# Performance work log

Hardware: AMD Instinct MI355X
Metric: run time of the kernel (lower is better)

Reference implementation:

```python
import jax, jax.numpy as jnp
import numpy as np

NUM_QUERIES = 300


def setup_inputs() -> dict:
    key = jax.random.key(0)
    ks = jax.random.split(key, 16)
    B, C, NC = 16, 256, 80
    s = 0.02
    return {
        "s3": jax.random.normal(ks[0], (B, C, 128, 128), jnp.float32),
        "s4": jax.random.normal(ks[1], (B, C, 64, 64), jnp.float32),
        "s5": jax.random.normal(ks[2], (B, C, 32, 32), jnp.float32),
        "w_score": jax.random.normal(ks[3], (C, NC), jnp.float32) * s,
        "b_score": jnp.zeros((NC,), jnp.float32),
        "w1": jax.random.normal(ks[4], (C, C), jnp.float32) * s,
        "b1": jnp.zeros((C,), jnp.float32),
        "w2": jax.random.normal(ks[5], (C, C), jnp.float32) * s,
        "b2": jnp.zeros((C,), jnp.float32),
        "w3": jax.random.normal(ks[6], (C, 4), jnp.float32) * s,
        "b3": jnp.zeros((4,), jnp.float32),
        "w_proj": jax.random.normal(ks[7], (C, C), jnp.float32) * s,
        "b_proj": jnp.zeros((C,), jnp.float32),
    }


def _flatten(feats):
    # each feat [B,C,H,W] -> [B,H*W,C]; concat over levels
    mems = [f.reshape(f.shape[0], f.shape[1], -1).transpose(0, 2, 1) for f in feats]
    return jnp.concatenate(mems, axis=1)


def reference(s3, s4, s5, w_score, b_score, w1, b1, w2, b2, w3, b3, w_proj, b_proj):
    memory = _flatten([s3, s4, s5])  # [B, N, C]

    # encoder heads
    enc_logits = memory @ w_score + b_score                      # [B, N, num_classes]
    h = jax.nn.relu(memory @ w1 + b1)
    h = jax.nn.relu(h @ w2 + b2)
    enc_boxes = h @ w3 + b3                                      # [B, N, 4]

    # top-k query selection: sigmoid -> per-token max class score -> topk -> gather
    scores = jax.nn.sigmoid(enc_logits).max(axis=-1)             # [B, N]
    topk_scores, topk_idx = jax.lax.top_k(scores, NUM_QUERIES)   # [B, K]
    topk_mem = jnp.take_along_axis(memory, topk_idx[:, :, None], axis=1)    # [B, K, C]
    topk_boxes = jnp.take_along_axis(enc_boxes, topk_idx[:, :, None], axis=1)  # [B, K, 4]

    tgt = topk_mem @ w_proj + b_proj                             # [B, K, C]
    ref_points = jax.nn.sigmoid(topk_boxes)                      # [B, K, 4]

    return (tgt, ref_points, enc_logits, jax.nn.sigmoid(enc_boxes), topk_idx, topk_scores)
```

## Files before the change

kernel.cpp:

```cpp
#include <hip/hip_runtime.h>
#include <math.h>

#define BATCH 16
#define CDIM 256
#define NCLS 80
#define N3 16384
#define N4 4096
#define N5 1024
#define NTOK 21504
#define KQ 300
#define KSEL 512
#define CANDMAX 1024

typedef __attribute__((ext_vector_type(8))) short short8;
typedef __attribute__((ext_vector_type(4))) float floatx4;
typedef unsigned short ushort_t;

__device__ __forceinline__ float sigmoidf_(float x) {
    return 1.0f / (1.0f + __expf(-x));
}

__device__ __forceinline__ ushort_t f2bf(float f) {
    unsigned int x = __float_as_uint(f);
    unsigned int r = (x + 0x7FFFu + ((x >> 16) & 1u)) >> 16;
    return (ushort_t)r;
}

__device__ __forceinline__ void gload16(const void* g, void* l) {
    __builtin_amdgcn_global_load_lds(
        (const __attribute__((address_space(1))) unsigned int*)g,
        (__attribute__((address_space(3))) unsigned int*)l,
        16, 0, 0);
}

__device__ __forceinline__ void locate_level(
    int n, int bb,
    const float* __restrict__ s3, const float* __restrict__ s4, const float* __restrict__ s5,
    const float*& src, int& nloc, int& lsz)
{
    if (n < N3)           { src = s3 + (size_t)bb * CDIM * N3; nloc = n;           lsz = N3; }
    else if (n < N3 + N4) { src = s4 + (size_t)bb * CDIM * N4; nloc = n - N3;      lsz = N4; }
    else                  { src = s5 + (size_t)bb * CDIM * N5; nloc = n - N3 - N4; lsz = N5; }
}

__global__ __launch_bounds__(256) void prep_weights(
    const float* __restrict__ w1, const float* __restrict__ w2,
    const float* __restrict__ w_score,
    ushort_t* __restrict__ w1T, ushort_t* __restrict__ w2T, ushort_t* __restrict__ wsT)
{
    const int k = threadIdx.x;
    const int c = blockIdx.x;
    const int klo = k & 7;
    if (c < 256) {
        const size_t d = (size_t)c * 256 + ((((k >> 3) ^ (c & 7)) << 3) | klo);
        w1T[d] = f2bf(w1[k * 256 + c]);
    } else if (c < 512) {
        const int c2 = c - 256;
        const size_t d = (size_t)c2 * 256 + ((((k >> 3) ^ (c2 & 7)) << 3) | klo);
        w2T[d] = f2bf(w2[k * 256 + c2]);
    } else {
        const int c2 = c - 512;
        const size_t d = (size_t)c2 * 256 + ((((k >> 3) ^ (c2 & 7)) << 3) | klo);
        wsT[d] = (c2 < NCLS) ? f2bf(w_score[k * NCLS + c2]) : (ushort_t)0;
    }
}

__global__ __launch_bounds__(256, 2) void enc_mfma_kernel(
    const float* __restrict__ s3, const float* __restrict__ s4, const float* __restrict__ s5,
    const ushort_t* __restrict__ w1T, const ushort_t* __restrict__ w2T,
    const ushort_t* __restrict__ wsT,
    const float* __restrict__ b_score, const float* __restrict__ b1,
    const float* __restrict__ b2,
    const float* __restrict__ w3, const float* __restrict__ b3,
    float* __restrict__ out_logits, float* __restrict__ out_sboxes,
    float* __restrict__ ws_scores)
{
    __shared__ __align__(16) ushort_t ldsA[256 * 68];
    __shared__ __align__(16) ushort_t wbufL[2][32 * 256];
    __shared__ float bsc_s[96];
    __shared__ float b1_s[256];
    __shared__ float b2_s[256];
    __shared__ __align__(16) float w3_s[256 * 4];

    const int t = threadIdx.x;
    const int lane = t & 63;
    const int w = t >> 6;
    const int ml = lane & 15;
    const int quad = lane >> 4;
    const int kq = quad * 8;
    const int m8 = ml & 7;

    const int bb = blockIdx.x / 336;
    const int tile = blockIdx.x % 336;
    const int T0 = tile * 64;

    auto stage_async = [&](const ushort_t* wg, int dbuf) {
        const char* g = (const char*)wg + w * 1024 + (lane << 4);
        char* l = (char*)&wbufL[dbuf][0] + w * 1024;
        #pragma unroll
        for (int i = 0; i < 4; ++i)
            gload16(g + i * 4096, l + i * 4096);
    };

    stage_async(wsT, 0);

    if (t < 96) bsc_s[t] = b_score[t];
    b1_s[t] = b1[t];
    b2_s[t] = b2[t];
    *(float4*)&w3_s[t * 4] = *(const float4*)(w3 + t * 4);

    const float* src; int nloc, lsz;
    locate_level(T0, bb, s3, s4, s5, src, nloc, lsz);

    {
        const int tokq = t & 15;
        const int kr = t >> 4;
        #pragma unroll
        for (int p = 0; p < 16; ++p) {
            const int k = p * 16 + kr;
            const float4 v = *(const float4*)(src + (size_t)k * lsz + nloc + 4 * tokq);
            const unsigned int lo = (unsigned int)f2bf(v.x) | ((unsigned int)f2bf(v.y) << 16);
            const unsigned int hi = (unsigned int)f2bf(v.z) | ((unsigned int)f2bf(v.w) << 16);
            *(uint2*)&ldsA[k * 68 + 4 * tokq] = make_uint2(lo, hi);
        }
    }
    __syncthreads();

    short8 af[8];
    #pragma unroll
    for (int f = 0; f < 8; ++f) {
        short8 a;
        #pragma unroll
        for (int j = 0; j < 8; ++j)
            a[j] = (short)ldsA[(32 * f + kq + j) * 68 + 16 * w + ml];
        af[f] = a;
    }

    const int tokl0 = 16 * w + quad * 4;
    const int tokg0 = bb * NTOK + T0 + tokl0;

    float smax[4] = {-1e30f, -1e30f, -1e30f, -1e30f};
    float psum[4][4];
    #pragma unroll
    for (int r = 0; r < 4; ++r)
        #pragma unroll
        for (int c = 0; c < 4; ++c) psum[r][c] = 0.f;

    int cur = 0;
    for (int i = 0; i < 19; ++i) {
        if (i + 1 < 19) {
            const int j = i + 1;
            const ushort_t* nxt = (j < 3)  ? (wsT + (size_t)j * 8192)
                                : (j < 11) ? (w1T + (size_t)(j - 3) * 8192)
                                           : (w2T + (size_t)(j - 11) * 8192);
            stage_async(nxt, cur ^ 1);
        }

        if (i == 11) {
            #pragma unroll
            for (int f = 0; f < 8; ++f)
                af[f] = *(const short8*)&ldsA[(16 * w + ml) * 264 + 32 * f + kq];
        }

        const ushort_t* wb = &wbufL[cur][0];
        #pragma unroll
        for (int tt = 0; tt < 2; ++tt) {
            if (i < 3 && (2 * i + tt) >= 5) continue;
            const int row = 16 * tt + ml;
            floatx4 acc = {0.f, 0.f, 0.f, 0.f};
            #pragma unroll
            for (int f = 0; f < 8; ++f) {
                const short8 bf = *(const short8*)&wb[row * 256 + (((4 * f + quad) ^ m8) << 3)];
                acc = __builtin_amdgcn_mfma_f32_16x16x32_bf16(af[f], bf, acc, 0, 0, 0);
            }
            if (i < 3) {
                const int col = 16 * (2 * i + tt) + ml;
                const float bias = bsc_s[col];
                #pragma unroll
                for (int r = 0; r < 4; ++r) {
                    const float v = acc[r] + bias;
                    out_logits[(size_t)(tokg0 + r) * NCLS + col] = v;
                    smax[r] = fmaxf(smax[r], v);
                }
            } else if (i < 11) {
                const int col = 32 * (i - 3) + 16 * tt + ml;
                const float bias = b1_s[col];
                #pragma unroll
                for (int r = 0; r < 4; ++r) {
                    const float v = fmaxf(acc[r] + bias, 0.f);
                    ldsA[(tokl0 + r) * 264 + col] = f2bf(v);
                }
            } else {
                const int col = 32 * (i - 11) + 16 * tt + ml;
                const float bias = b2_s[col];
                const float4 w3v = *(const float4*)&w3_s[col * 4];
                #pragma unroll
                for (int r = 0; r < 4; ++r) {
                    const float v = fmaxf(acc[r] + bias, 0.f);
                    psum[r][0] = fmaf(v, w3v.x, psum[r][0]);
                    psum[r][1] = fmaf(v, w3v.y, psum[r][1]);
                    psum[r][2] = fmaf(v, w3v.z, psum[r][2]);
                    psum[r][3] = fmaf(v, w3v.w, psum[r][3]);
                }
            }
        }

        if (i == 2) {
            #pragma unroll
            for (int r = 0; r < 4; ++r) {
                float m = smax[r];
                m = fmaxf(m, __shfl_xor(m, 1));
                m = fmaxf(m, __shfl_xor(m, 2));
                m = fmaxf(m, __shfl_xor(m, 4));
                m = fmaxf(m, __shfl_xor(m, 8));
                smax[r] = m;
            }
            if (ml == 0) {
                #pragma unroll
                for (int r = 0; r < 4; ++r)
                    ws_scores[bb * NTOK + T0 + 16 * w + quad * 4 + r] = sigmoidf_(smax[r]);
            }
        }

        __syncthreads();
        cur ^= 1;
    }

    #pragma unroll
    for (int r = 0; r < 4; ++r)
        #pragma unroll
        for (int c = 0; c < 4; ++c) {
            float v = psum[r][c];
            v += __shfl_xor(v, 1);
            v += __shfl_xor(v, 2);
            v += __shfl_xor(v, 4);
            v += __shfl_xor(v, 8);
            psum[r][c] = v;
        }
    if (ml == 0) {
        #pragma unroll
        for (int r = 0; r < 4; ++r) {
            float4 o;
            o.x = sigmoidf_(psum[r][0] + b3[0]);
            o.y = sigmoidf_(psum[r][1] + b3[1]);
            o.z = sigmoidf_(psum[r][2] + b3[2]);
            o.w = sigmoidf_(psum[r][3] + b3[3]);
            *(float4*)&out_sboxes[(size_t)(bb * NTOK + T0 + 16 * w + quad * 4 + r) * 4] = o;
        }
    }
}

__global__ __launch_bounds__(1024) void select_kernel(
    const float* __restrict__ scores,
    int* __restrict__ cand_idx, unsigned int* __restrict__ cand_cnt)
{
    const int bb = blockIdx.x;
    const int t = threadIdx.x;
    const int lane = t & 63;
    const float* s = scores + bb * NTOK;

    __shared__ unsigned int hist[256];
    __shared__ unsigned int prefix_s, rem_s, cnt_s;

    unsigned int prefix = 0, mask = 0;
    int remaining = KSEL;
    for (int pass = 0; pass < 4; pass++) {
        const int shift = 24 - 8 * pass;
        if (t < 256) hist[t] = 0;
        __syncthreads();
        for (int n = t; n < NTOK; n += 1024) {
            const unsigned int key = __float_as_uint(s[n]);
            const bool pred = ((key & mask) == prefix);
            const unsigned int bin = (key >> shift) & 255u;
            unsigned long long alive = __ballot(pred);
            while (alive) {
                const int leader = __builtin_ctzll(alive);
                const unsigned int lbin = (unsigned int)__shfl((int)bin, leader);
                const unsigned long long match = alive & __ballot(bin == lbin);
                if (lane == leader)
                    atomicAdd(&hist[lbin], (unsigned int)__popcll(match));
                alive &= ~match;
            }
        }
        __syncthreads();
        if (t == 0) {
            int rem = remaining; unsigned int bsel = 0;
            for (int bin = 255; bin >= 0; bin--) {
                int c = (int)hist[bin];
                if (c >= rem) { bsel = (unsigned int)bin; break; }
                rem -= c;
            }
            prefix_s = prefix | (bsel << shift);
            rem_s = (unsigned int)rem;
        }
        __syncthreads();
        prefix = prefix_s; remaining = (int)rem_s;
        mask |= 0xFFu << shift;
        __syncthreads();
    }
    const unsigned int Tkey = prefix;

    if (t == 0) cnt_s = 0;
    __syncthreads();
    for (int n = t; n < NTOK; n += 1024) {
        const unsigned int key = __float_as_uint(s[n]);
        const bool pred = (key >= Tkey);
        const unsigned long long m = __ballot(pred);
        if (m) {
            const int leader = __builtin_ctzll(m);
            unsigned int base = 0;
            if (lane == leader) base = atomicAdd(&cnt_s, (unsigned int)__popcll(m));
            base = (unsigned int)__shfl((int)base, leader);
            if (pred) {
                const unsigned int pos =
                    base + (unsigned int)__popcll(m & ((1ull << lane) - 1ull));
                if (pos < CANDMAX) cand_idx[bb * CANDMAX + pos] = n;
            }
        }
    }
    __syncthreads();
    if (t == 0) {
        unsigned int c = cnt_s; if (c > CANDMAX) c = CANDMAX;
        cand_cnt[bb] = c;
    }
}

__global__ __launch_bounds__(256) void rescore_kernel(
    const float* __restrict__ s3, const float* __restrict__ s4, const float* __restrict__ s5,
    const float* __restrict__ w_score, const float* __restrict__ b_score,
    const int* __restrict__ cand_idx, const unsigned int* __restrict__ cand_cnt,
    double* __restrict__ cand_score)
{
    __shared__ float mrow[4][CDIM];
    const int t = threadIdx.x;
    const int w = t >> 6;
    const int lane = t & 63;
    const int bb = blockIdx.x / (CANDMAX / 4);
    const int c  = (blockIdx.x % (CANDMAX / 4)) * 4 + w;
    const unsigned int cnt = cand_cnt[bb];
    const bool active = (unsigned int)c < cnt;

    int n = 0;
    if (active) n = cand_idx[bb * CANDMAX + c];
    if (active) {
        const float* src; int nloc, lsz;
        locate_level(n, bb, s3, s4, s5, src, nloc, lsz);
        #pragma unroll
        for (int j = 0; j < 4; j++)
            mrow[w][4 * lane + j] = src[(size_t)(4 * lane + j) * lsz + nloc];
    }
    __syncthreads();

    if (active) {
        double acc0 = (double)b_score[lane];
        double acc1 = (lane < 16) ? (double)b_score[64 + lane] : -1.0e300;
        for (int k = 0; k < CDIM; k++) {
            const double m = (double)mrow[w][k];
            acc0 += m * (double)w_score[k * NCLS + lane];
            if (lane < 16) acc1 += m * (double)w_score[k * NCLS + 64 + lane];
        }
        double mx = fmax(acc0, acc1);
        mx = fmax(mx, __shfl_xor(mx, 1));
        mx = fmax(mx, __shfl_xor(mx, 2));
        mx = fmax(mx, __shfl_xor(mx, 4));
        mx = fmax(mx, __shfl_xor(mx, 8));
        mx = fmax(mx, __shfl_xor(mx, 16));
        mx = fmax(mx, __shfl_xor(mx, 32));
        if (lane == 0) cand_score[bb * CANDMAX + c] = mx;
    }
}

__global__ __launch_bounds__(256) void fsort_kernel(
    const double* __restrict__ cand_score, const int* __restrict__ cand_idx,
    const unsigned int* __restrict__ cand_cnt,
    float* __restrict__ out_idx_f, float* __restrict__ out_scores,
    int* __restrict__ ws_idx)
{
    __shared__ double ss[CANDMAX];
    __shared__ int    ii[CANDMAX];
    const int bb = blockIdx.x;
    const int t = threadIdx.x;
    const unsigned int cnt = cand_cnt[bb];

    for (int i = t; i < CANDMAX; i += 256) {
        if ((unsigned int)i < cnt) {
            ss[i] = cand_score[bb * CANDMAX + i];
            ii[i] = cand_idx[bb * CANDMAX + i];
        } else {
            ss[i] = -1.0e300;
            ii[i] = 0x7FFFFFFF;
        }
    }
    __syncthreads();

    for (int ksz = 2; ksz <= CANDMAX; ksz <<= 1) {
        for (int j = ksz >> 1; j > 0; j >>= 1) {
            #pragma unroll
            for (int p = 0; p < CANDMAX / 256; p++) {
                const int i = p * 256 + t;
                const int ixj = i ^ j;
                if (ixj > i) {
                    double sa = ss[i], sb = ss[ixj];
                    int ia = ii[i], ib = ii[ixj];
                    const bool up = ((i & ksz) != 0);
                    const bool agtb = (sa > sb) || (sa == sb && ia < ib);
                    if (agtb == up) { ss[i] = sb; ss[ixj] = sa; ii[i] = ib; ii[ixj] = ia; }
                }
            }
            __syncthreads();
        }
    }

    for (int q = t; q < KQ; q += 256) {
        const double x = ss[q];
        const int idx = ii[q];
        out_scores[bb * KQ + q] = (float)(1.0 / (1.0 + exp(-x)));
        out_idx_f[bb * KQ + q] = (float)idx;
        ws_idx[bb * KQ + q] = idx;
    }
}

__global__ __launch_bounds__(256) void gather_proj_kernel(
    const float* __restrict__ s3, const float* __restrict__ s4, const float* __restrict__ s5,
    const float* __restrict__ w_proj, const float* __restrict__ b_proj,
    const int* __restrict__ ws_idx, const float* __restrict__ out_sboxes,
    float* __restrict__ out_tgt, float* __restrict__ out_ref)
{
    __shared__ float memQ[20][CDIM];
    __shared__ int qidx[20];
    const int t = threadIdx.x;
    const int bb = blockIdx.x / 15;
    const int tile = blockIdx.x % 15;
    const int q0 = tile * 20;

    if (t < 20) qidx[t] = ws_idx[bb * KQ + q0 + t];
    __syncthreads();

    #pragma unroll 4
    for (int q = 0; q < 20; q++) {
        const int n = qidx[q];
        const float* src; int nloc, lsz;
        locate_level(n, bb, s3, s4, s5, src, nloc, lsz);
        memQ[q][t] = src[(size_t)t * lsz + nloc];
    }
    __syncthreads();

    const int j = t;
    float acc[20];
    #pragma unroll
    for (int q = 0; q < 20; q++) acc[q] = b_proj[j];
    for (int k = 0; k < CDIM; k++) {
        const float w = w_proj[(size_t)k * CDIM + j];
        #pragma unroll
        for (int q = 0; q < 20; q++) acc[q] = fmaf(memQ[q][k], w, acc[q]);
    }
    #pragma unroll
    for (int q = 0; q < 20; q++)
        out_tgt[(size_t)(bb * KQ + q0 + q) * CDIM + j] = acc[q];

    if (t < 80) {
        const int q = t >> 2, c = t & 3;
        const int n = qidx[q];
        out_ref[(size_t)(bb * KQ + q0 + q) * 4 + c] =
            out_sboxes[(size_t)(bb * NTOK + n) * 4 + c];
    }
}

extern "C" void kernel_launch(void* const* d_in, const int* in_sizes, int n_in,
                              void* d_out, int out_size, void* d_ws, size_t ws_size,
                              hipStream_t stream) {
    const float* s3      = (const float*)d_in[0];
    const float* s4      = (const float*)d_in[1];
    const float* s5      = (const float*)d_in[2];
    const float* w_score = (const float*)d_in[3];
    const float* b_score = (const float*)d_in[4];
    const float* w1      = (const float*)d_in[5];
    const float* b1      = (const float*)d_in[6];
    const float* w2      = (const float*)d_in[7];
    const float* b2      = (const float*)d_in[8];
    const float* w3      = (const float*)d_in[9];
    const float* b3      = (const float*)d_in[10];
    const float* w_proj  = (const float*)d_in[11];
    const float* b_proj  = (const float*)d_in[12];

    float* out = (float*)d_out;
    float* out_tgt    = out;
    float* out_ref    = out + 1228800;
    float* out_logits = out + 1248000;
    float* out_sboxes = out + 28773120;
    float* out_idx    = out + 30149376;
    float* out_scores = out + 30154176;

    char* ws = (char*)d_ws;
    float*        ws_scores  = (float*)(ws + 0);
    double*       cand_score = (double*)(ws + 1376256);
    int*          cand_idx   = (int*)(ws + 1507328);
    unsigned int* cand_cnt   = (unsigned int*)(ws + 1572864);
    int*          ws_idx     = (int*)(ws + 1573120);
    ushort_t*     w1T        = (ushort_t*)(ws + 1592576);
    ushort_t*     w2T        = (ushort_t*)(ws + 1723648);
    ushort_t*     wsT        = (ushort_t*)(ws + 1854720);

    prep_weights<<<608, 256, 0, stream>>>(w1, w2, w_score, w1T, w2T, wsT);

    enc_mfma_kernel<<<BATCH * 336, 256, 0, stream>>>(
        s3, s4, s5, w1T, w2T, wsT, b_score, b1, b2, w3, b3,
        out_logits, out_sboxes, ws_scores);

    select_kernel<<<BATCH, 1024, 0, stream>>>(ws_scores, cand_idx, cand_cnt);

    rescore_kernel<<<BATCH * (CANDMAX / 4), 256, 0, stream>>>(
        s3, s4, s5, w_score, b_score, cand_idx, cand_cnt, cand_score);

    fsort_kernel<<<BATCH, 256, 0, stream>>>(
        cand_score, cand_idx, cand_cnt, out_idx, out_scores, ws_idx);

    gather_proj_kernel<<<BATCH * 15, 256, 0, stream>>>(
        s3, s4, s5, w_proj, b_proj, ws_idx, out_sboxes, out_tgt, out_ref);
}
```

Baseline: 956.4 us.

## Restructure encoder MLP to 32x32 MFMA with direct global weight fragments

The encoder kernel moves from 16x16x32 MFMA tiles with double-buffered LDS weight staging and per-step barriers to 32x32x16 MFMA tiles. Weights are pre-packed into MFMA fragment order and read straight from global/L2 memory, and the four waves split into two token halves by two column groups. The box head becomes a separate LDS pass after layer two, and select_kernel drops from 1024 to 256 threads with a simpler histogram update. This removes LDS weight staging and many syncs, but every block now re-reads weights from global memory and the register footprint grows.

```diff
diff --git a/kernel.cpp b/kernel.cpp
--- a/kernel.cpp
+++ b/kernel.cpp
@@ -14,6 +14,7 @@
 
 typedef __attribute__((ext_vector_type(8))) short short8;
 typedef __attribute__((ext_vector_type(4))) float floatx4;
+typedef __attribute__((ext_vector_type(16))) float floatx16;
 typedef unsigned short ushort_t;
 
 __device__ __forceinline__ float sigmoidf_(float x) {
@@ -26,11 +27,8 @@
     return (ushort_t)r;
 }
 
-__device__ __forceinline__ void gload16(const void* g, void* l) {
-    __builtin_amdgcn_global_load_lds(
-        (const __attribute__((address_space(1))) unsigned int*)g,
-        (__attribute__((address_space(3))) unsigned int*)l,
-        16, 0, 0);
+__device__ __forceinline__ float bf2f(ushort_t u) {
+    return __uint_as_float((unsigned int)u << 16);
 }
 
 __device__ __forceinline__ void locate_level(
@@ -46,29 +44,32 @@
 __global__ __launch_bounds__(256) void prep_weights(
     const float* __restrict__ w1, const float* __restrict__ w2,
     const float* __restrict__ w_score,
-    ushort_t* __restrict__ w1T, ushort_t* __restrict__ w2T, ushort_t* __restrict__ wsT)
-{
-    const int k = threadIdx.x;
+    ushort_t* __restrict__ wPk)
+{
     const int c = blockIdx.x;
-    const int klo = k & 7;
-    if (c < 256) {
-        const size_t d = (size_t)c * 256 + ((((k >> 3) ^ (c & 7)) << 3) | klo);
-        w1T[d] = f2bf(w1[k * 256 + c]);
-    } else if (c < 512) {
-        const int c2 = c - 256;
-        const size_t d = (size_t)c2 * 256 + ((((k >> 3) ^ (c2 & 7)) << 3) | klo);
-        w2T[d] = f2bf(w2[k * 256 + c2]);
-    } else {
-        const int c2 = c - 512;
-        const size_t d = (size_t)c2 * 256 + ((((k >> 3) ^ (c2 & 7)) << 3) | klo);
-        wsT[d] = (c2 < NCLS) ? f2bf(w_score[k * NCLS + c2]) : (ushort_t)0;
-    }
-}
-
-__global__ __launch_bounds__(256, 2) void enc_mfma_kernel(
+    for (int i = threadIdx.x; i < 8192; i += 256) {
+        const int f = i >> 9;
+        const int e = i & 511;
+        const int ln = e >> 3;
+        const int j = e & 7;
+        const int col = ln & 31;
+        const int k = 16 * f + (ln >> 5) * 8 + j;
+        float v;
+        if (c < 3) {
+            const int cc = 32 * c + col;
+            v = (cc < NCLS) ? w_score[k * NCLS + cc] : 0.f;
+        } else if (c < 11) {
+            v = w1[k * 256 + (32 * (c - 3) + col)];
+        } else {
+            v = w2[k * 256 + (32 * (c - 11) + col)];
+        }
+        wPk[(size_t)c * 8192 + i] = f2bf(v);
+    }
+}
+
+__global__ __launch_bounds__(256) void enc_mfma_kernel(
     const float* __restrict__ s3, const float* __restrict__ s4, const float* __restrict__ s5,
-    const ushort_t* __restrict__ w1T, const ushort_t* __restrict__ w2T,
-    const ushort_t* __restrict__ wsT,
+    const ushort_t* __restrict__ wPk,
     const float* __restrict__ b_score, const float* __restrict__ b1,
     const float* __restrict__ b2,
     const float* __restrict__ w3, const float* __restrict__ b3,
@@ -76,38 +77,20 @@
     float* __restrict__ ws_scores)
 {
     __shared__ __align__(16) ushort_t ldsA[256 * 68];
-    __shared__ __align__(16) ushort_t wbufL[2][32 * 256];
-    __shared__ float bsc_s[96];
-    __shared__ float b1_s[256];
-    __shared__ float b2_s[256];
     __shared__ __align__(16) float w3_s[256 * 4];
+    __shared__ float smax_s[2][64];
 
     const int t = threadIdx.x;
     const int lane = t & 63;
     const int w = t >> 6;
-    const int ml = lane & 15;
-    const int quad = lane >> 4;
-    const int kq = quad * 8;
-    const int m8 = ml & 7;
+    const int tw = w & 1;
+    const int cw = w >> 1;
+    const int ln = lane & 31;
+    const int half = lane >> 5;
 
     const int bb = blockIdx.x / 336;
     const int tile = blockIdx.x % 336;
     const int T0 = tile * 64;
-
-    auto stage_async = [&](const ushort_t* wg, int dbuf) {
-        const char* g = (const char*)wg + w * 1024 + (lane << 4);
-        char* l = (char*)&wbufL[dbuf][0] + w * 1024;
-        #pragma unroll
-        for (int i = 0; i < 4; ++i)
-            gload16(g + i * 4096, l + i * 4096);
-    };
-
-    stage_async(wsT, 0);
-
-    if (t < 96) bsc_s[t] = b_score[t];
-    b1_s[t] = b1[t];
-    b2_s[t] = b2[t];
-    *(float4*)&w3_s[t * 4] = *(const float4*)(w3 + t * 4);
 
     const float* src; int nloc, lsz;
     locate_level(T0, bb, s3, s4, s5, src, nloc, lsz);
@@ -123,134 +106,137 @@
             const unsigned int hi = (unsigned int)f2bf(v.z) | ((unsigned int)f2bf(v.w) << 16);
             *(uint2*)&ldsA[k * 68 + 4 * tokq] = make_uint2(lo, hi);
         }
-    }
-    __syncthreads();
-
-    short8 af[8];
+        *(float4*)&w3_s[t * 4] = *(const float4*)(w3 + t * 4);
+    }
+    __syncthreads();
+
+    short8 af[16];
     #pragma unroll
-    for (int f = 0; f < 8; ++f) {
+    for (int f = 0; f < 16; ++f) {
         short8 a;
         #pragma unroll
         for (int j = 0; j < 8; ++j)
-            a[j] = (short)ldsA[(32 * f + kq + j) * 68 + 16 * w + ml];
+            a[j] = (short)ldsA[(16 * f + 8 * half + j) * 68 + 32 * tw + ln];
         af[f] = a;
     }
-
-    const int tokl0 = 16 * w + quad * 4;
-    const int tokg0 = bb * NTOK + T0 + tokl0;
-
-    float smax[4] = {-1e30f, -1e30f, -1e30f, -1e30f};
-    float psum[4][4];
+    __syncthreads();
+
+    const int gtok0 = bb * NTOK + T0 + 32 * tw;
+
+    float smaxr[16];
     #pragma unroll
-    for (int r = 0; r < 4; ++r)
-        #pragma unroll
-        for (int c = 0; c < 4; ++c) psum[r][c] = 0.f;
-
-    int cur = 0;
-    for (int i = 0; i < 19; ++i) {
-        if (i + 1 < 19) {
-            const int j = i + 1;
-            const ushort_t* nxt = (j < 3)  ? (wsT + (size_t)j * 8192)
-                                : (j < 11) ? (w1T + (size_t)(j - 3) * 8192)
-                                           : (w2T + (size_t)(j - 11) * 8192);
-            stage_async(nxt, cur ^ 1);
-        }
-
-        if (i == 11) {
-            #pragma unroll
-            for (int f = 0; f < 8; ++f)
-                af[f] = *(const short8*)&ldsA[(16 * w + ml) * 264 + 32 * f + kq];
-        }
-
-        const ushort_t* wb = &wbufL[cur][0];
-        #pragma unroll
-        for (int tt = 0; tt < 2; ++tt) {
-            if (i < 3 && (2 * i + tt) >= 5) continue;
-            const int row = 16 * tt + ml;
-            floatx4 acc = {0.f, 0.f, 0.f, 0.f};
-            #pragma unroll
-            for (int f = 0; f < 8; ++f) {
-                const short8 bf = *(const short8*)&wb[row * 256 + (((4 * f + quad) ^ m8) << 3)];
-                acc = __builtin_amdgcn_mfma_f32_16x16x32_bf16(af[f], bf, acc, 0, 0, 0);
-            }
-            if (i < 3) {
-                const int col = 16 * (2 * i + tt) + ml;
-                const float bias = bsc_s[col];
-                #pragma unroll
-                for (int r = 0; r < 4; ++r) {
-                    const float v = acc[r] + bias;
-                    out_logits[(size_t)(tokg0 + r) * NCLS + col] = v;
-                    smax[r] = fmaxf(smax[r], v);
-                }
-            } else if (i < 11) {
-                const int col = 32 * (i - 3) + 16 * tt + ml;
-                const float bias = b1_s[col];
-                #pragma unroll
-                for (int r = 0; r < 4; ++r) {
-                    const float v = fmaxf(acc[r] + bias, 0.f);
-                    ldsA[(tokl0 + r) * 264 + col] = f2bf(v);
-                }
-            } else {
-                const int col = 32 * (i - 11) + 16 * tt + ml;
-                const float bias = b2_s[col];
-                const float4 w3v = *(const float4*)&w3_s[col * 4];
-                #pragma unroll
-                for (int r = 0; r < 4; ++r) {
-                    const float v = fmaxf(acc[r] + bias, 0.f);
-                    psum[r][0] = fmaf(v, w3v.x, psum[r][0]);
-                    psum[r][1] = fmaf(v, w3v.y, psum[r][1]);
-                    psum[r][2] = fmaf(v, w3v.z, psum[r][2]);
-                    psum[r][3] = fmaf(v, w3v.w, psum[r][3]);
+    for (int r = 0; r < 16; ++r) smaxr[r] = -1e30f;
+
+    for (int c = cw; c < 11; c += 2) {
+        const ushort_t* bp = wPk + (size_t)c * 8192;
+        floatx16 acc = {0.f,0.f,0.f,0.f,0.f,0.f,0.f,0.f,0.f,0.f,0.f,0.f,0.f,0.f,0.f,0.f};
+        #pragma unroll
+        for (int fh = 0; fh < 2; ++fh) {
+            short8 bf[8];
+            #pragma unroll
+            for (int f2 = 0; f2 < 8; ++f2)
+                bf[f2] = *(const short8*)&bp[(8 * fh + f2) * 512 + lane * 8];
+            #pragma unroll
+            for (int f2 = 0; f2 < 8; ++f2)
+                acc = __builtin_amdgcn_mfma_f32_32x32x16_bf16(af[8 * fh + f2], bf[f2], acc, 0, 0, 0);
+        }
+        if (c < 3) {
+            const int col = 32 * c + ln;
+            const bool valid = col < NCLS;
+            const float bias = valid ? b_score[col] : 0.f;
+            #pragma unroll
+            for (int r = 0; r < 16; ++r) {
+                const int row = (r & 3) + 8 * (r >> 2) + 4 * half;
+                const float v = acc[r] + bias;
+                if (valid) {
+                    out_logits[(size_t)(gtok0 + row) * NCLS + col] = v;
+                    smaxr[r] = fmaxf(smaxr[r], v);
                 }
             }
-        }
-
-        if (i == 2) {
-            #pragma unroll
-            for (int r = 0; r < 4; ++r) {
-                float m = smax[r];
-                m = fmaxf(m, __shfl_xor(m, 1));
-                m = fmaxf(m, __shfl_xor(m, 2));
-                m = fmaxf(m, __shfl_xor(m, 4));
-                m = fmaxf(m, __shfl_xor(m, 8));
-                smax[r] = m;
+        } else {
+            const int col = 32 * (c - 3) + ln;
+            const float bias = b1[col];
+            #pragma unroll
+            for (int r = 0; r < 16; ++r) {
+                const int row = (r & 3) + 8 * (r >> 2) + 4 * half;
+                const int tok = 32 * tw + row;
+                const float v = fmaxf(acc[r] + bias, 0.f);
+                ldsA[tok * 256 + ((((col >> 3) ^ (row & 7)) << 3) | (col & 7))] = f2bf(v);
             }
-            if (ml == 0) {
-                #pragma unroll
-                for (int r = 0; r < 4; ++r)
-                    ws_scores[bb * NTOK + T0 + 16 * w + quad * 4 + r] = sigmoidf_(smax[r]);
-            }
-        }
-
-        __syncthreads();
-        cur ^= 1;
+        }
     }
 
     #pragma unroll
-    for (int r = 0; r < 4; ++r)
-        #pragma unroll
-        for (int c = 0; c < 4; ++c) {
-            float v = psum[r][c];
-            v += __shfl_xor(v, 1);
-            v += __shfl_xor(v, 2);
-            v += __shfl_xor(v, 4);
-            v += __shfl_xor(v, 8);
-            psum[r][c] = v;
-        }
-    if (ml == 0) {
-        #pragma unroll
-        for (int r = 0; r < 4; ++r) {
-            float4 o;
-            o.x = sigmoidf_(psum[r][0] + b3[0]);
-            o.y = sigmoidf_(psum[r][1] + b3[1]);
-            o.z = sigmoidf_(psum[r][2] + b3[2]);
-            o.w = sigmoidf_(psum[r][3] + b3[3]);
-            *(float4*)&out_sboxes[(size_t)(bb * NTOK + T0 + 16 * w + quad * 4 + r) * 4] = o;
-        }
-    }
-}
-
-__global__ __launch_bounds__(1024) void select_kernel(
+    for (int r = 0; r < 16; ++r) {
+        float m = smaxr[r];
+        m = fmaxf(m, __shfl_xor(m, 1));
+        m = fmaxf(m, __shfl_xor(m, 2));
+        m = fmaxf(m, __shfl_xor(m, 4));
+        m = fmaxf(m, __shfl_xor(m, 8));
+        m = fmaxf(m, __shfl_xor(m, 16));
+        if (ln == 0) {
+            const int row = (r & 3) + 8 * (r >> 2) + 4 * half;
+            smax_s[cw][32 * tw + row] = m;
+        }
+    }
+    __syncthreads();
+
+    if (t < 64) {
+        const float m = fmaxf(smax_s[0][t], smax_s[1][t]);
+        ws_scores[bb * NTOK + T0 + t] = sigmoidf_(m);
+    }
+
+    {
+        const int tok = 32 * tw + ln;
+        #pragma unroll
+        for (int f = 0; f < 16; ++f) {
+            const int chnk = 2 * f + half;
+            af[f] = *(const short8*)&ldsA[tok * 256 + ((chnk ^ (tok & 7)) << 3)];
+        }
+    }
+    __syncthreads();
+
+    for (int c = 11 + cw; c < 19; c += 2) {
+        const ushort_t* bp = wPk + (size_t)c * 8192;
+        floatx16 acc = {0.f,0.f,0.f,0.f,0.f,0.f,0.f,0.f,0.f,0.f,0.f,0.f,0.f,0.f,0.f,0.f};
+        #pragma unroll
+        for (int fh = 0; fh < 2; ++fh) {
+            short8 bf[8];
+            #pragma unroll
+            for (int f2 = 0; f2 < 8; ++f2)
+                bf[f2] = *(const short8*)&bp[(8 * fh + f2) * 512 + lane * 8];
+            #pragma unroll
+            for (int f2 = 0; f2 < 8; ++f2)
+                acc = __builtin_amdgcn_mfma_f32_32x32x16_bf16(af[8 * fh + f2], bf[f2], acc, 0, 0, 0);
+        }
+        const int col = 32 * (c - 11) + ln;
+        const float bias = b2[col];
+        #pragma unroll
+        for (int r = 0; r < 16; ++r) {
+            const int row = (r & 3) + 8 * (r >> 2) + 4 * half;
+            const int tok = 32 * tw + row;
+            const float v = fmaxf(acc[r] + bias, 0.f);
+            ldsA[tok * 256 + ((((col >> 3) ^ (row & 7)) << 3) | (col & 7))] = f2bf(v);
+        }
+    }
+    __syncthreads();
+
+    {
+        const int tok = t >> 2;
+        const int j = t & 3;
+        float acc = b3[j];
+        #pragma unroll
+        for (int ch = 0; ch < 32; ++ch) {
+            const short8 v = *(const short8*)&ldsA[tok * 256 + ((ch ^ (tok & 7)) << 3)];
+            #pragma unroll
+            for (int jj = 0; jj < 8; ++jj)
+                acc = fmaf(bf2f((ushort_t)v[jj]), w3_s[(ch * 8 + jj) * 4 + j], acc);
+        }
+        out_sboxes[(size_t)(bb * NTOK + T0 + tok) * 4 + j] = sigmoidf_(acc);
+    }
+}
+
+__global__ __launch_bounds__(256) void select_kernel(
     const float* __restrict__ scores,
     int* __restrict__ cand_idx, unsigned int* __restrict__ cand_cnt)
 {
@@ -266,20 +252,21 @@
     int remaining = KSEL;
     for (int pass = 0; pass < 4; pass++) {
         const int shift = 24 - 8 * pass;
-        if (t < 256) hist[t] = 0;
+        hist[t] = 0;
         __syncthreads();
-        for (int n = t; n < NTOK; n += 1024) {
+        for (int n = t; n < NTOK; n += 256) {
             const unsigned int key = __float_as_uint(s[n]);
             const bool pred = ((key & mask) == prefix);
-            const unsigned int bin = (key >> shift) & 255u;
-            unsigned long long alive = __ballot(pred);
-            while (alive) {
+            const unsigned int bin = pred ? ((key >> shift) & 255u) : 0xFFFFu;
+            const unsigned long long alive = __ballot(pred);
+            if (alive) {
                 const int leader = __builtin_ctzll(alive);
                 const unsigned int lbin = (unsigned int)__shfl((int)bin, leader);
-                const unsigned long long match = alive & __ballot(bin == lbin);
+                const unsigned long long match = __ballot(pred && bin == lbin);
                 if (lane == leader)
                     atomicAdd(&hist[lbin], (unsigned int)__popcll(match));
-                alive &= ~match;
+                else if (pred && bin != lbin)
+                    atomicAdd(&hist[bin], 1u);
             }
         }
         __syncthreads();
@@ -302,7 +289,7 @@
 
     if (t == 0) cnt_s = 0;
     __syncthreads();
-    for (int n = t; n < NTOK; n += 1024) {
+    for (int n = t; n < NTOK; n += 256) {
         const unsigned int key = __float_as_uint(s[n]);
         const bool pred = (key >= Tkey);
         const unsigned long long m = __ballot(pred);
@@ -497,17 +484,15 @@
     int*          cand_idx   = (int*)(ws + 1507328);
     unsigned int* cand_cnt   = (unsigned int*)(ws + 1572864);
     int*          ws_idx     = (int*)(ws + 1573120);
-    ushort_t*     w1T        = (ushort_t*)(ws + 1592576);
-    ushort_t*     w2T        = (ushort_t*)(ws + 1723648);
-    ushort_t*     wsT        = (ushort_t*)(ws + 1854720);
-
-    prep_weights<<<608, 256, 0, stream>>>(w1, w2, w_score, w1T, w2T, wsT);
+    ushort_t*     wPk        = (ushort_t*)(ws + 1592576);
+
+    prep_weights<<<19, 256, 0, stream>>>(w1, w2, w_score, wPk);
 
     enc_mfma_kernel<<<BATCH * 336, 256, 0, stream>>>(
-        s3, s4, s5, w1T, w2T, wsT, b_score, b1, b2, w3, b3,
+        s3, s4, s5, wPk, b_score, b1, b2, w3, b3,
         out_logits, out_sboxes, ws_scores);
 
-    select_kernel<<<BATCH, 1024, 0, stream>>>(ws_scores, cand_idx, cand_cnt);
+    select_kernel<<<BATCH, 256, 0, stream>>>(ws_scores, cand_idx, cand_cnt);
 
     rescore_kernel<<<BATCH * (CANDMAX / 4), 256, 0, stream>>>(
         s3, s4, s5, w_score, b_score, cand_idx, cand_cnt, cand_score);
```

New measurement: 1.038 ms. +8.5%, slower.

## Restructure top-k tail: one candidate per block, cache candidate rows, wider sort

Applied to the files above, without the earlier changes.

The rescore kernel now gives each candidate its own 256-thread block, so all threads take part in the row gather and the work is split into two K-halves. When the workspace is large enough it also writes the gathered row to a cand_mem buffer. The sort carries the original candidate position, which lets gather_proj read contiguous cached rows instead of doing strided gathers from the feature maps again. The select kernel drops to 256 threads and replaces the loop-until-done histogram aggregation with a single leader aggregation plus per-lane atomics. Use of the cache depends on workspace size, and the extra 16 MB buffer adds write traffic.

```diff
diff --git a/kernel.cpp b/kernel.cpp
--- a/kernel.cpp
+++ b/kernel.cpp
@@ -250,7 +250,7 @@
     }
 }
 
-__global__ __launch_bounds__(1024) void select_kernel(
+__global__ __launch_bounds__(256) void select_kernel(
     const float* __restrict__ scores,
     int* __restrict__ cand_idx, unsigned int* __restrict__ cand_cnt)
 {
@@ -266,20 +266,21 @@
     int remaining = KSEL;
     for (int pass = 0; pass < 4; pass++) {
         const int shift = 24 - 8 * pass;
-        if (t < 256) hist[t] = 0;
+        hist[t] = 0;
         __syncthreads();
-        for (int n = t; n < NTOK; n += 1024) {
+        for (int n = t; n < NTOK; n += 256) {
             const unsigned int key = __float_as_uint(s[n]);
             const bool pred = ((key & mask) == prefix);
-            const unsigned int bin = (key >> shift) & 255u;
-            unsigned long long alive = __ballot(pred);
-            while (alive) {
+            const unsigned int bin = pred ? ((key >> shift) & 255u) : 0xFFFFu;
+            const unsigned long long alive = __ballot(pred);
+            if (alive) {
                 const int leader = __builtin_ctzll(alive);
                 const unsigned int lbin = (unsigned int)__shfl((int)bin, leader);
-                const unsigned long long match = alive & __ballot(bin == lbin);
+                const unsigned long long match = __ballot(pred && bin == lbin);
                 if (lane == leader)
                     atomicAdd(&hist[lbin], (unsigned int)__popcll(match));
-                alive &= ~match;
+                else if (pred && bin != lbin)
+                    atomicAdd(&hist[bin], 1u);
             }
         }
         __syncthreads();
@@ -302,7 +303,7 @@
 
     if (t == 0) cnt_s = 0;
     __syncthreads();
-    for (int n = t; n < NTOK; n += 1024) {
+    for (int n = t; n < NTOK; n += 256) {
         const unsigned int key = __float_as_uint(s[n]);
         const bool pred = (key >= Tkey);
         const unsigned long long m = __ballot(pred);
@@ -329,60 +330,69 @@
     const float* __restrict__ s3, const float* __restrict__ s4, const float* __restrict__ s5,
     const float* __restrict__ w_score, const float* __restrict__ b_score,
     const int* __restrict__ cand_idx, const unsigned int* __restrict__ cand_cnt,
-    double* __restrict__ cand_score)
-{
-    __shared__ float mrow[4][CDIM];
+    double* __restrict__ cand_score, float* __restrict__ cand_mem, int use_cmem)
+{
+    __shared__ float m_s[CDIM];
+    __shared__ double part[256];
+
     const int t = threadIdx.x;
-    const int w = t >> 6;
-    const int lane = t & 63;
-    const int bb = blockIdx.x / (CANDMAX / 4);
-    const int c  = (blockIdx.x % (CANDMAX / 4)) * 4 + w;
-    const unsigned int cnt = cand_cnt[bb];
-    const bool active = (unsigned int)c < cnt;
-
-    int n = 0;
-    if (active) n = cand_idx[bb * CANDMAX + c];
-    if (active) {
-        const float* src; int nloc, lsz;
-        locate_level(n, bb, s3, s4, s5, src, nloc, lsz);
-        #pragma unroll
-        for (int j = 0; j < 4; j++)
-            mrow[w][4 * lane + j] = src[(size_t)(4 * lane + j) * lsz + nloc];
-    }
-    __syncthreads();
-
-    if (active) {
-        double acc0 = (double)b_score[lane];
-        double acc1 = (lane < 16) ? (double)b_score[64 + lane] : -1.0e300;
-        for (int k = 0; k < CDIM; k++) {
-            const double m = (double)mrow[w][k];
-            acc0 += m * (double)w_score[k * NCLS + lane];
-            if (lane < 16) acc1 += m * (double)w_score[k * NCLS + 64 + lane];
-        }
-        double mx = fmax(acc0, acc1);
-        mx = fmax(mx, __shfl_xor(mx, 1));
-        mx = fmax(mx, __shfl_xor(mx, 2));
-        mx = fmax(mx, __shfl_xor(mx, 4));
-        mx = fmax(mx, __shfl_xor(mx, 8));
-        mx = fmax(mx, __shfl_xor(mx, 16));
-        mx = fmax(mx, __shfl_xor(mx, 32));
-        if (lane == 0) cand_score[bb * CANDMAX + c] = mx;
-    }
-}
-
-__global__ __launch_bounds__(256) void fsort_kernel(
+    const int bb = blockIdx.x / CANDMAX;
+    const int cpos = blockIdx.x % CANDMAX;
+    if ((unsigned int)cpos >= cand_cnt[bb]) return;
+
+    const int n = cand_idx[bb * CANDMAX + cpos];
+    const float* src; int nloc, lsz;
+    locate_level(n, bb, s3, s4, s5, src, nloc, lsz);
+    m_s[t] = src[(size_t)t * lsz + nloc];
+    __syncthreads();
+
+    if (use_cmem)
+        cand_mem[((size_t)bb * CANDMAX + cpos) * CDIM + t] = m_s[t];
+
+    const int ks = t >> 7;
+    const int c = t & 127;
+    double acc = 0.0;
+    if (c < NCLS) {
+        if (ks == 0) acc = (double)b_score[c];
+        const int k0 = 128 * ks;
+        for (int k = k0; k < k0 + 128; ++k)
+            acc += (double)m_s[k] * (double)w_score[k * NCLS + c];
+    }
+    part[t] = acc;
+    __syncthreads();
+
+    if (t < 128) {
+        double tot = (t < NCLS) ? (part[t] + part[t + 128]) : -1.0e300;
+        part[t] = tot;
+    }
+    __syncthreads();
+
+    if (t < 64) {
+        double v = fmax(part[t], part[t + 64]);
+        v = fmax(v, __shfl_xor(v, 1));
+        v = fmax(v, __shfl_xor(v, 2));
+        v = fmax(v, __shfl_xor(v, 4));
+        v = fmax(v, __shfl_xor(v, 8));
+        v = fmax(v, __shfl_xor(v, 16));
+        v = fmax(v, __shfl_xor(v, 32));
+        if (t == 0) cand_score[bb * CANDMAX + cpos] = v;
+    }
+}
+
+__global__ __launch_bounds__(512) void fsort_kernel(
     const double* __restrict__ cand_score, const int* __restrict__ cand_idx,
     const unsigned int* __restrict__ cand_cnt,
     float* __restrict__ out_idx_f, float* __restrict__ out_scores,
-    int* __restrict__ ws_idx)
+    int* __restrict__ ws_idx, int* __restrict__ ws_pos)
 {
     __shared__ double ss[CANDMAX];
     __shared__ int    ii[CANDMAX];
+    __shared__ int    pp[CANDMAX];
     const int bb = blockIdx.x;
     const int t = threadIdx.x;
     const unsigned int cnt = cand_cnt[bb];
 
-    for (int i = t; i < CANDMAX; i += 256) {
+    for (int i = t; i < CANDMAX; i += 512) {
         if ((unsigned int)i < cnt) {
             ss[i] = cand_score[bb * CANDMAX + i];
             ii[i] = cand_idx[bb * CANDMAX + i];
@@ -390,58 +400,76 @@
             ss[i] = -1.0e300;
             ii[i] = 0x7FFFFFFF;
         }
+        pp[i] = i;
     }
     __syncthreads();
 
     for (int ksz = 2; ksz <= CANDMAX; ksz <<= 1) {
         for (int j = ksz >> 1; j > 0; j >>= 1) {
             #pragma unroll
-            for (int p = 0; p < CANDMAX / 256; p++) {
-                const int i = p * 256 + t;
+            for (int p = 0; p < CANDMAX / 512; p++) {
+                const int i = p * 512 + t;
                 const int ixj = i ^ j;
                 if (ixj > i) {
                     double sa = ss[i], sb = ss[ixj];
                     int ia = ii[i], ib = ii[ixj];
                     const bool up = ((i & ksz) != 0);
                     const bool agtb = (sa > sb) || (sa == sb && ia < ib);
-                    if (agtb == up) { ss[i] = sb; ss[ixj] = sa; ii[i] = ib; ii[ixj] = ia; }
+                    if (agtb == up) {
+                        ss[i] = sb; ss[ixj] = sa;
+                        ii[i] = ib; ii[ixj] = ia;
+                        const int pa = pp[i]; pp[i] = pp[ixj]; pp[ixj] = pa;
+                    }
                 }
             }
             __syncthreads();
         }
     }
 
-    for (int q = t; q < KQ; q += 256) {
+    for (int q = t; q < KQ; q += 512) {
         const double x = ss[q];
         const int idx = ii[q];
         out_scores[bb * KQ + q] = (float)(1.0 / (1.0 + exp(-x)));
         out_idx_f[bb * KQ + q] = (float)idx;
         ws_idx[bb * KQ + q] = idx;
+        ws_pos[bb * KQ + q] = pp[q];
     }
 }
 
 __global__ __launch_bounds__(256) void gather_proj_kernel(
     const float* __restrict__ s3, const float* __restrict__ s4, const float* __restrict__ s5,
     const float* __restrict__ w_proj, const float* __restrict__ b_proj,
-    const int* __restrict__ ws_idx, const float* __restrict__ out_sboxes,
+    const int* __restrict__ ws_idx, const int* __restrict__ ws_pos,
+    const float* __restrict__ cand_mem, int use_cmem,
+    const float* __restrict__ out_sboxes,
     float* __restrict__ out_tgt, float* __restrict__ out_ref)
 {
     __shared__ float memQ[20][CDIM];
     __shared__ int qidx[20];
+    __shared__ int qpos[20];
     const int t = threadIdx.x;
     const int bb = blockIdx.x / 15;
     const int tile = blockIdx.x % 15;
     const int q0 = tile * 20;
 
-    if (t < 20) qidx[t] = ws_idx[bb * KQ + q0 + t];
-    __syncthreads();
-
-    #pragma unroll 4
-    for (int q = 0; q < 20; q++) {
-        const int n = qidx[q];
-        const float* src; int nloc, lsz;
-        locate_level(n, bb, s3, s4, s5, src, nloc, lsz);
-        memQ[q][t] = src[(size_t)t * lsz + nloc];
+    if (t < 20) {
+        qidx[t] = ws_idx[bb * KQ + q0 + t];
+        qpos[t] = ws_pos[bb * KQ + q0 + t];
+    }
+    __syncthreads();
+
+    if (use_cmem) {
+        #pragma unroll 4
+        for (int q = 0; q < 20; q++)
+            memQ[q][t] = cand_mem[((size_t)bb * CANDMAX + qpos[q]) * CDIM + t];
+    } else {
+        #pragma unroll 4
+        for (int q = 0; q < 20; q++) {
+            const int n = qidx[q];
+            const float* src; int nloc, lsz;
+            locate_level(n, bb, s3, s4, s5, src, nloc, lsz);
+            memQ[q][t] = src[(size_t)t * lsz + nloc];
+        }
     }
     __syncthreads();
 
@@ -497,9 +525,12 @@
     int*          cand_idx   = (int*)(ws + 1507328);
     unsigned int* cand_cnt   = (unsigned int*)(ws + 1572864);
     int*          ws_idx     = (int*)(ws + 1573120);
-    ushort_t*     w1T        = (ushort_t*)(ws + 1592576);
-    ushort_t*     w2T        = (ushort_t*)(ws + 1723648);
-    ushort_t*     wsT        = (ushort_t*)(ws + 1854720);
+    int*          ws_pos     = (int*)(ws + 1592576);
+    ushort_t*     w1T        = (ushort_t*)(ws + 1612032);
+    ushort_t*     w2T        = (ushort_t*)(ws + 1743104);
+    ushort_t*     wsT        = (ushort_t*)(ws + 1874176);
+    float*        cand_mem   = (float*)(ws + 1923328);
+    const int use_cmem = (ws_size >= (size_t)1923328 + 16777216) ? 1 : 0;
 
     prep_weights<<<608, 256, 0, stream>>>(w1, w2, w_score, w1T, w2T, wsT);
 
@@ -507,14 +538,16 @@
         s3, s4, s5, w1T, w2T, wsT, b_score, b1, b2, w3, b3,
         out_logits, out_sboxes, ws_scores);
 
-    select_kernel<<<BATCH, 1024, 0, stream>>>(ws_scores, cand_idx, cand_cnt);
-
-    rescore_kernel<<<BATCH * (CANDMAX / 4), 256, 0, stream>>>(
-        s3, s4, s5, w_score, b_score, cand_idx, cand_cnt, cand_score);
-
-    fsort_kernel<<<BATCH, 256, 0, stream>>>(
-        cand_score, cand_idx, cand_cnt, out_idx, out_scores, ws_idx);
+    select_kernel<<<BATCH, 256, 0, stream>>>(ws_scores, cand_idx, cand_cnt);
+
+    rescore_kernel<<<BATCH * CANDMAX, 256, 0, stream>>>(
+        s3, s4, s5, w_score, b_score, cand_idx, cand_cnt,
+        cand_score, cand_mem, use_cmem);
+
+    fsort_kernel<<<BATCH, 512, 0, stream>>>(
+        cand_score, cand_idx, cand_cnt, out_idx, out_scores, ws_idx, ws_pos);
 
     gather_proj_kernel<<<BATCH * 15, 256, 0, stream>>>(
-        s3, s4, s5, w_proj, b_proj, ws_idx, out_sboxes, out_tgt, out_ref);
-}
+        s3, s4, s5, w_proj, b_proj, ws_idx, ws_pos, cand_mem, use_cmem,
+        out_sboxes, out_tgt, out_ref);
+}
```

New measurement: 1.020 ms. +6.6%, slower.
